# Kernel tuning notes

Hardware: AMD Instinct MI355X
Metric: run time of the kernel (lower is better)

Reference implementation:

```python
import jax, jax.numpy as jnp
import numpy as np

B, T, I, H, O = 4096, 256, 5, 64, 25


def _lstm_layer(x, Wih, Whh, bih, bhh):
    """One LSTM layer, batch_first. x: [B,T,in], Wih: [4H,in], Whh: [4H,H].
    PyTorch gate order: i, f, g, o."""
    b, t, _ = x.shape
    h_dim = Whh.shape[1]
    # Precompute input contribution for all timesteps: [B,T,4H]
    gx = jnp.einsum('bti,gi->btg', x, Wih) + bih + bhh

    def step(carry, g_t):
        h, c = carry
        gates = g_t + h @ Whh.T  # [B,4H]
        i, f, g, o = jnp.split(gates, 4, axis=-1)
        i = jax.nn.sigmoid(i)
        f = jax.nn.sigmoid(f)
        g = jnp.tanh(g)
        o = jax.nn.sigmoid(o)
        c = f * c + i * g
        h = o * jnp.tanh(c)
        return (h, c), h

    h0 = jnp.zeros((b, h_dim), x.dtype)
    (_, _), hs = jax.lax.scan(step, (h0, h0), jnp.swapaxes(gx, 0, 1))  # hs: [T,B,H]
    return jnp.swapaxes(hs, 0, 1)  # [B,T,H]


def setup_inputs() -> dict:
    key = jax.random.key(0)
    ks = jax.random.split(key, 12)
    k = 1.0 / np.sqrt(H)  # torch LSTM/Linear init scale
    u = lambda kk, shp: jax.random.uniform(kk, shp, jnp.float32, -k, k)
    return {
        'x': jax.random.normal(ks[0], (B, T, I), jnp.float32),
        'Wih0': u(ks[1], (4 * H, I)),
        'Whh0': u(ks[2], (4 * H, H)),
        'bih0': u(ks[3], (4 * H,)),
        'bhh0': u(ks[4], (4 * H,)),
        'Wih1': u(ks[5], (4 * H, H)),
        'Whh1': u(ks[6], (4 * H, H)),
        'bih1': u(ks[7], (4 * H,)),
        'bhh1': u(ks[8], (4 * H,)),
        'Wfc': u(ks[9], (O, H)),
        'bfc': u(ks[10], (O,)),
    }


def reference(x, Wih0, Whh0, bih0, bhh0, Wih1, Whh1, bih1, bhh1, Wfc, bfc):
    # 2-layer LSTM (dropout = identity in eval mode)
    h1 = _lstm_layer(x, Wih0, Whh0, bih0, bhh0)   # [B,T,H]
    h2 = _lstm_layer(h1, Wih1, Whh1, bih1, bhh1)  # [B,T,H]
    last = h2[:, -1, :]                            # [B,H]
    out = last @ Wfc.T + bfc                       # [B,25]
    return out.reshape(x.shape[0], 5, 5)
```

## Files before the change

### kernel.cpp

```cpp
#include <hip/hip_runtime.h>


#define TT   256
#define II   5
#define HH   64
#define OO   25
#define MT   16
#define NTHR 1024
#define XP   520
#define HSZ  1024
#define HF   65

typedef __attribute__((ext_vector_type(8))) short  short8;
typedef __attribute__((ext_vector_type(4))) float  floatx4;

#define MFMA(a, b, c) __builtin_amdgcn_mfma_f32_16x16x32_bf16(a, b, c, 0, 0, 0)

__device__ __forceinline__ float frcp(float x) { return __builtin_amdgcn_rcpf(x); }
__device__ __forceinline__ float fexp2(float x) { return __builtin_amdgcn_exp2f(x); }
__device__ __forceinline__ unsigned short bf16_rne(float f) {
    unsigned int u = __builtin_bit_cast(unsigned int, f);
    u += 0x7FFFu + ((u >> 16) & 1u);
    return (unsigned short)(u >> 16);
}
__device__ __forceinline__ float cell_update(const floatx4& g, float& c) {
    const float gi = frcp(1.f + fexp2(g[0]));
    const float gf = frcp(1.f + fexp2(g[1]));
    const float gz = fmaf(-2.f, frcp(1.f + fexp2(g[2])), 1.f);
    const float go = frcp(1.f + fexp2(g[3]));
    c = fmaf(gf, c, gi * gz);
    const float tc = fmaf(-2.f, frcp(1.f + fexp2(c * 2.885390082f)), 1.f);
    return go * tc;
}

__global__ __attribute__((amdgpu_flat_work_group_size(1024, 1024),
                          amdgpu_waves_per_eu(4, 4)))
void lstm_mfma9(const float* __restrict__ x,
                const float* __restrict__ Wih0, const float* __restrict__ Whh0,
                const float* __restrict__ bih0, const float* __restrict__ bhh0,
                const float* __restrict__ Wih1, const float* __restrict__ Whh1,
                const float* __restrict__ bih1, const float* __restrict__ bhh1,
                const float* __restrict__ Wfc,  const float* __restrict__ bfc,
                float* __restrict__ out)
{
    __shared__ __align__(16) unsigned short xhi[MT * XP];
    __shared__ __align__(16) unsigned short h1hi[2 * HSZ];
    __shared__ __align__(16) unsigned short h2hi[2 * HSZ];
    __shared__ __align__(16) float          h2f[MT * HF];

    const int tid   = threadIdx.x;
    const int w     = tid >> 6;
    const int lane  = tid & 63;
    const int b     = lane & 15;
    const int q     = lane >> 4;
    const int jmine = 4 * w + q;
    const int hw_off = ((jmine >> 3) * 16 + b) * 8 + (jmine & 7);
    const int ro     = lane * 8;

    short8 A1h[2];
    short8 A2h[4];
    short8 Axwh;
    {
        const int rr = lane & 15;
        const int g  = (rr & 3) * 64 + 4 * w + (rr >> 2);
        const float sc = ((rr & 3) == 2) ? 2.885390082f : -1.442695041f;
        #pragma unroll
        for (int c = 0; c < 2; ++c)
            #pragma unroll
            for (int jj = 0; jj < 8; ++jj)
                A1h[c][jj] = (short)bf16_rne(sc * Whh0[g * HH + c * 32 + q * 8 + jj]);
        #pragma unroll
        for (int c = 0; c < 4; ++c)
            #pragma unroll
            for (int jj = 0; jj < 8; ++jj) {
                const int k = c * 32 + q * 8 + jj;
                float wv = (k < HH) ? Wih1[g * HH + k] : Whh1[g * HH + (k - HH)];
                A2h[c][jj] = (short)bf16_rne(sc * wv);
            }
        #pragma unroll
        for (int jj = 0; jj < 8; ++jj) {
            const int k = q * 8 + jj;
            Axwh[jj] = (k < II) ? (short)bf16_rne(sc * Wih0[g * II + k]) : (short)0;
        }
    }
    float bias1[4], bias2[4];
    #pragma unroll
    for (int r = 0; r < 4; ++r) {
        const int g = r * 64 + jmine;
        const float sc = (r == 2) ? 2.885390082f : -1.442695041f;
        bias1[r] = sc * (bih0[g] + bhh0[g]);
        bias2[r] = sc * (bih1[g] + bhh1[g]);
    }

    for (int i = tid; i < MT * XP / 2; i += NTHR)
        ((unsigned int*)xhi)[i] = 0u;
    for (int i = tid; i < HSZ; i += NTHR) {
        ((unsigned int*)h1hi)[i] = 0u;
        ((unsigned int*)h2hi)[i] = 0u;
    }
    float c1 = 0.f, c2 = 0.f;
    __syncthreads();

    const int blockBase = blockIdx.x * MT;

    auto refill_x = [&](int t0) {
        const int rb = tid >> 6, dt = tid & 63;
        const float* src = x + ((size_t)(blockBase + rb) * TT + t0 + dt) * II;
        unsigned short* ph = xhi + rb * XP + dt * 8;
        #pragma unroll
        for (int ii = 0; ii < II; ++ii)
            ph[ii] = bf16_rne(src[ii]);
    };

    refill_x(0);
    __syncthreads();
    {
        short8 Bxh = *(const short8*)(xhi + b * XP);
        floatx4 a1 = {bias1[0], bias1[1], bias1[2], bias1[3]};
        a1 = MFMA(Axwh, Bxh, a1);
        const float h = cell_update(a1, c1);
        h1hi[0 * HSZ + hw_off] = bf16_rne(h);
    }
    __syncthreads();

    const unsigned short* xptr = xhi + b * XP + 8;

#define STEP_BODY(WP, RP)                                                     \
    {                                                                         \
        short8 H1h0 = *(const short8*)(h1hi + (WP) * HSZ + ro);               \
        short8 H1h1 = *(const short8*)(h1hi + (WP) * HSZ + 512 + ro);         \
        short8 H2h0 = *(const short8*)(h2hi + (RP) * HSZ + ro);               \
        short8 H2h1 = *(const short8*)(h2hi + (RP) * HSZ + 512 + ro);         \
        short8 Bxh  = *(const short8*)(xptr);                                 \
        xptr += 8;                                                            \
        floatx4 a2 = {bias2[0], bias2[1], bias2[2], bias2[3]};                \
        a2 = MFMA(A2h[0], H1h0, a2);                                          \
        a2 = MFMA(A2h[1], H1h1, a2);                                          \
        a2 = MFMA(A2h[2], H2h0, a2);                                          \
        a2 = MFMA(A2h[3], H2h1, a2);                                          \
        floatx4 a1 = {bias1[0], bias1[1], bias1[2], bias1[3]};                \
        a1 = MFMA(Axwh, Bxh, a1);                                             \
        a1 = MFMA(A1h[0], H1h0, a1);                                          \
        a1 = MFMA(A1h[1], H1h1, a1);                                          \
        {                                                                     \
            const float h = cell_update(a2, c2);                              \
            h2hi[(WP) * HSZ + hw_off] = bf16_rne(h);                          \
        }                                                                     \
        {                                                                     \
            const float h = cell_update(a1, c1);                              \
            h1hi[(RP) * HSZ + hw_off] = bf16_rne(h);                          \
        }                                                                     \
        __syncthreads();                                                      \
    }

    for (int i = 0; i < 254; i += 2) {
        STEP_BODY(0, 1)
        if (((i + 2) & 63) == 0) {
            refill_x(i + 2);
            xptr = xhi + b * XP;
            __syncthreads();
        }
        STEP_BODY(1, 0)
    }
    STEP_BODY(0, 1)
#undef STEP_BODY

    {
        short8 H1h0 = *(const short8*)(h1hi + 1 * HSZ + ro);
        short8 H1h1 = *(const short8*)(h1hi + 1 * HSZ + 512 + ro);
        short8 H2h0 = *(const short8*)(h2hi + 0 * HSZ + ro);
        short8 H2h1 = *(const short8*)(h2hi + 0 * HSZ + 512 + ro);
        floatx4 a2 = {bias2[0], bias2[1], bias2[2], bias2[3]};
        a2 = MFMA(A2h[0], H1h0, a2);
        a2 = MFMA(A2h[1], H1h1, a2);
        a2 = MFMA(A2h[2], H2h0, a2);
        a2 = MFMA(A2h[3], H2h1, a2);
        const float h = cell_update(a2, c2);
        h2f[b * HF + jmine] = h;
    }
    __syncthreads();

    if (tid < MT * OO) {
        const int bb = tid / OO, o = tid - bb * OO;
        float acc = bfc[o];
        const float* wr = Wfc + o * HH;
        const float* hr = h2f + bb * HF;
        #pragma unroll
        for (int j = 0; j < HH; ++j) acc += wr[j] * hr[j];
        out[((size_t)blockIdx.x * MT + bb) * OO + o] = acc;
    }
}

extern "C" void kernel_launch(void* const* d_in, const int* in_sizes, int n_in,
                              void* d_out, int out_size, void* d_ws, size_t ws_size,
                              hipStream_t stream) {
    const float* x    = (const float*)d_in[0];
    const float* Wih0 = (const float*)d_in[1];
    const float* Whh0 = (const float*)d_in[2];
    const float* bih0 = (const float*)d_in[3];
    const float* bhh0 = (const float*)d_in[4];
    const float* Wih1 = (const float*)d_in[5];
    const float* Whh1 = (const float*)d_in[6];
    const float* bih1 = (const float*)d_in[7];
    const float* bhh1 = (const float*)d_in[8];
    const float* Wfc  = (const float*)d_in[9];
    const float* bfc  = (const float*)d_in[10];
    float* out = (float*)d_out;

    dim3 grid(4096 / MT), block(NTHR);
    lstm_mfma9<<<grid, block, 0, stream>>>(x, Wih0, Whh0, bih0, bhh0,
                                           Wih1, Whh1, bih1, bhh1,
                                           Wfc, bfc, out);
}
```

Measured before the change: 259.8 us.

## Halve batch tile per block and give each wave two gate tiles

Shrinks each block to 8 batch rows and 512 threads, doubling the grid, so a CU can host two independent blocks whose recurrences interleave. Each wave now owns 8 hidden units and issues two interleaved MFMA chains. The 16-wide MFMA B operand carries the 8 batch rows twice, and each hidden value is written to both copies. The aim is cheaper 512-thread barriers and better latency hiding across blocks, in exchange for doubling total MFMA work, since half of each output tile is redundant.

```diff
diff --git a/kernel.cpp b/kernel.cpp
--- a/kernel.cpp
+++ b/kernel.cpp
@@ -5,8 +5,8 @@
 #define II   5
 #define HH   64
 #define OO   25
-#define MT   16
-#define NTHR 1024
+#define MT   8
+#define NTHR 512
 #define XP   520
 #define HSZ  1024
 #define HF   65
@@ -33,15 +33,15 @@
     return go * tc;
 }
 
-__global__ __attribute__((amdgpu_flat_work_group_size(1024, 1024),
+__global__ __attribute__((amdgpu_flat_work_group_size(512, 512),
                           amdgpu_waves_per_eu(4, 4)))
-void lstm_mfma9(const float* __restrict__ x,
-                const float* __restrict__ Wih0, const float* __restrict__ Whh0,
-                const float* __restrict__ bih0, const float* __restrict__ bhh0,
-                const float* __restrict__ Wih1, const float* __restrict__ Whh1,
-                const float* __restrict__ bih1, const float* __restrict__ bhh1,
-                const float* __restrict__ Wfc,  const float* __restrict__ bfc,
-                float* __restrict__ out)
+void lstm_mfma10(const float* __restrict__ x,
+                 const float* __restrict__ Wih0, const float* __restrict__ Whh0,
+                 const float* __restrict__ bih0, const float* __restrict__ bhh0,
+                 const float* __restrict__ Wih1, const float* __restrict__ Whh1,
+                 const float* __restrict__ bih1, const float* __restrict__ bhh1,
+                 const float* __restrict__ Wfc,  const float* __restrict__ bfc,
+                 float* __restrict__ out)
 {
     __shared__ __align__(16) unsigned short xhi[MT * XP];
     __shared__ __align__(16) unsigned short h1hi[2 * HSZ];
@@ -51,45 +51,50 @@
     const int tid   = threadIdx.x;
     const int w     = tid >> 6;
     const int lane  = tid & 63;
-    const int b     = lane & 15;
+    const int b8    = lane & 7;
     const int q     = lane >> 4;
-    const int jmine = 4 * w + q;
-    const int hw_off = ((jmine >> 3) * 16 + b) * 8 + (jmine & 7);
-    const int ro     = lane * 8;
-
-    short8 A1h[2];
-    short8 A2h[4];
-    short8 Axwh;
+    const int sel   = (lane >> 3) & 1;
+    const bool low  = (sel == 0);
+    const int jmine = 8 * w + 4 * sel + q;
+    const int hw_off = w * 128 + b8 * 8 + 4 * sel + q;
+    const int ro8    = (q * 16 + b8) * 8;
+
+    short8 A1h[2][2];
+    short8 A2h[2][4];
+    short8 Axwh[2];
     {
         const int rr = lane & 15;
-        const int g  = (rr & 3) * 64 + 4 * w + (rr >> 2);
         const float sc = ((rr & 3) == 2) ? 2.885390082f : -1.442695041f;
         #pragma unroll
-        for (int c = 0; c < 2; ++c)
+        for (int s = 0; s < 2; ++s) {
+            const int g = (rr & 3) * 64 + 8 * w + 4 * s + (rr >> 2);
             #pragma unroll
-            for (int jj = 0; jj < 8; ++jj)
-                A1h[c][jj] = (short)bf16_rne(sc * Whh0[g * HH + c * 32 + q * 8 + jj]);
-        #pragma unroll
-        for (int c = 0; c < 4; ++c)
+            for (int c = 0; c < 2; ++c)
+                #pragma unroll
+                for (int jj = 0; jj < 8; ++jj)
+                    A1h[s][c][jj] = (short)bf16_rne(sc * Whh0[g * HH + c * 32 + q * 8 + jj]);
+            #pragma unroll
+            for (int c = 0; c < 4; ++c)
+                #pragma unroll
+                for (int jj = 0; jj < 8; ++jj) {
+                    const int k = c * 32 + q * 8 + jj;
+                    float wv = (k < HH) ? Wih1[g * HH + k] : Whh1[g * HH + (k - HH)];
+                    A2h[s][c][jj] = (short)bf16_rne(sc * wv);
+                }
             #pragma unroll
             for (int jj = 0; jj < 8; ++jj) {
-                const int k = c * 32 + q * 8 + jj;
-                float wv = (k < HH) ? Wih1[g * HH + k] : Whh1[g * HH + (k - HH)];
-                A2h[c][jj] = (short)bf16_rne(sc * wv);
+                const int k = q * 8 + jj;
+                Axwh[s][jj] = (k < II) ? (short)bf16_rne(sc * Wih0[g * II + k]) : (short)0;
             }
-        #pragma unroll
-        for (int jj = 0; jj < 8; ++jj) {
-            const int k = q * 8 + jj;
-            Axwh[jj] = (k < II) ? (short)bf16_rne(sc * Wih0[g * II + k]) : (short)0;
         }
     }
-    float bias1[4], bias2[4];
+    floatx4 bias1v, bias2v;
     #pragma unroll
     for (int r = 0; r < 4; ++r) {
         const int g = r * 64 + jmine;
         const float sc = (r == 2) ? 2.885390082f : -1.442695041f;
-        bias1[r] = sc * (bih0[g] + bhh0[g]);
-        bias2[r] = sc * (bih1[g] + bhh1[g]);
+        bias1v[r] = sc * (bih0[g] + bhh0[g]);
+        bias2v[r] = sc * (bih1[g] + bhh1[g]);
     }
 
     for (int i = tid; i < MT * XP / 2; i += NTHR)
@@ -115,40 +120,59 @@
     refill_x(0);
     __syncthreads();
     {
-        short8 Bxh = *(const short8*)(xhi + b * XP);
-        floatx4 a1 = {bias1[0], bias1[1], bias1[2], bias1[3]};
-        a1 = MFMA(Axwh, Bxh, a1);
-        const float h = cell_update(a1, c1);
-        h1hi[0 * HSZ + hw_off] = bf16_rne(h);
-    }
-    __syncthreads();
-
-    const unsigned short* xptr = xhi + b * XP + 8;
+        short8 Bxh = *(const short8*)(xhi + b8 * XP);
+        floatx4 a1t0 = MFMA(Axwh[0], Bxh, bias1v);
+        floatx4 a1t1 = MFMA(Axwh[1], Bxh, bias1v);
+        floatx4 a1m;
+        #pragma unroll
+        for (int r = 0; r < 4; ++r) a1m[r] = low ? a1t0[r] : a1t1[r];
+        const float h = cell_update(a1m, c1);
+        const unsigned short hv = bf16_rne(h);
+        h1hi[0 * HSZ + hw_off]      = hv;
+        h1hi[0 * HSZ + hw_off + 64] = hv;
+    }
+    __syncthreads();
+
+    const unsigned short* xptr = xhi + b8 * XP + 8;
 
 #define STEP_BODY(WP, RP)                                                     \
     {                                                                         \
-        short8 H1h0 = *(const short8*)(h1hi + (WP) * HSZ + ro);               \
-        short8 H1h1 = *(const short8*)(h1hi + (WP) * HSZ + 512 + ro);         \
-        short8 H2h0 = *(const short8*)(h2hi + (RP) * HSZ + ro);               \
-        short8 H2h1 = *(const short8*)(h2hi + (RP) * HSZ + 512 + ro);         \
+        short8 H1h0 = *(const short8*)(h1hi + (WP) * HSZ + ro8);              \
+        short8 H1h1 = *(const short8*)(h1hi + (WP) * HSZ + 512 + ro8);        \
+        short8 H2h0 = *(const short8*)(h2hi + (RP) * HSZ + ro8);              \
+        short8 H2h1 = *(const short8*)(h2hi + (RP) * HSZ + 512 + ro8);        \
         short8 Bxh  = *(const short8*)(xptr);                                 \
         xptr += 8;                                                            \
-        floatx4 a2 = {bias2[0], bias2[1], bias2[2], bias2[3]};                \
-        a2 = MFMA(A2h[0], H1h0, a2);                                          \
-        a2 = MFMA(A2h[1], H1h1, a2);                                          \
-        a2 = MFMA(A2h[2], H2h0, a2);                                          \
-        a2 = MFMA(A2h[3], H2h1, a2);                                          \
-        floatx4 a1 = {bias1[0], bias1[1], bias1[2], bias1[3]};                \
-        a1 = MFMA(Axwh, Bxh, a1);                                             \
-        a1 = MFMA(A1h[0], H1h0, a1);                                          \
-        a1 = MFMA(A1h[1], H1h1, a1);                                          \
+        floatx4 a2t0 = MFMA(A2h[0][0], H1h0, bias2v);                         \
+        floatx4 a2t1 = MFMA(A2h[1][0], H1h0, bias2v);                         \
+        a2t0 = MFMA(A2h[0][1], H1h1, a2t0);                                   \
+        a2t1 = MFMA(A2h[1][1], H1h1, a2t1);                                   \
+        a2t0 = MFMA(A2h[0][2], H2h0, a2t0);                                   \
+        a2t1 = MFMA(A2h[1][2], H2h0, a2t1);                                   \
+        a2t0 = MFMA(A2h[0][3], H2h1, a2t0);                                   \
+        a2t1 = MFMA(A2h[1][3], H2h1, a2t1);                                   \
+        floatx4 a1t0 = MFMA(Axwh[0], Bxh, bias1v);                            \
+        floatx4 a1t1 = MFMA(Axwh[1], Bxh, bias1v);                            \
+        a1t0 = MFMA(A1h[0][0], H1h0, a1t0);                                   \
+        a1t1 = MFMA(A1h[1][0], H1h0, a1t1);                                   \
+        a1t0 = MFMA(A1h[0][1], H1h1, a1t0);                                   \
+        a1t1 = MFMA(A1h[1][1], H1h1, a1t1);                                   \
+        floatx4 a2m, a1m;                                                     \
+        _Pragma("unroll")                                                     \
+        for (int r = 0; r < 4; ++r) a2m[r] = low ? a2t0[r] : a2t1[r];         \
+        _Pragma("unroll")                                                     \
+        for (int r = 0; r < 4; ++r) a1m[r] = low ? a1t0[r] : a1t1[r];         \
         {                                                                     \
-            const float h = cell_update(a2, c2);                              \
-            h2hi[(WP) * HSZ + hw_off] = bf16_rne(h);                          \
+            const float h = cell_update(a2m, c2);                             \
+            const unsigned short hv = bf16_rne(h);                            \
+            h2hi[(WP) * HSZ + hw_off]      = hv;                              \
+            h2hi[(WP) * HSZ + hw_off + 64] = hv;                              \
         }                                                                     \
         {                                                                     \
-            const float h = cell_update(a1, c1);                              \
-            h1hi[(RP) * HSZ + hw_off] = bf16_rne(h);                          \
+            const float h = cell_update(a1m, c1);                             \
+            const unsigned short hv = bf16_rne(h);                            \
+            h1hi[(RP) * HSZ + hw_off]      = hv;                              \
+            h1hi[(RP) * HSZ + hw_off + 64] = hv;                              \
         }                                                                     \
         __syncthreads();                                                      \
     }
@@ -157,7 +181,7 @@
         STEP_BODY(0, 1)
         if (((i + 2) & 63) == 0) {
             refill_x(i + 2);
-            xptr = xhi + b * XP;
+            xptr = xhi + b8 * XP;
             __syncthreads();
         }
         STEP_BODY(1, 0)
@@ -166,17 +190,23 @@
 #undef STEP_BODY
 
     {
-        short8 H1h0 = *(const short8*)(h1hi + 1 * HSZ + ro);
-        short8 H1h1 = *(const short8*)(h1hi + 1 * HSZ + 512 + ro);
-        short8 H2h0 = *(const short8*)(h2hi + 0 * HSZ + ro);
-        short8 H2h1 = *(const short8*)(h2hi + 0 * HSZ + 512 + ro);
-        floatx4 a2 = {bias2[0], bias2[1], bias2[2], bias2[3]};
-        a2 = MFMA(A2h[0], H1h0, a2);
-        a2 = MFMA(A2h[1], H1h1, a2);
-        a2 = MFMA(A2h[2], H2h0, a2);
-        a2 = MFMA(A2h[3], H2h1, a2);
-        const float h = cell_update(a2, c2);
-        h2f[b * HF + jmine] = h;
+        short8 H1h0 = *(const short8*)(h1hi + 1 * HSZ + ro8);
+        short8 H1h1 = *(const short8*)(h1hi + 1 * HSZ + 512 + ro8);
+        short8 H2h0 = *(const short8*)(h2hi + 0 * HSZ + ro8);
+        short8 H2h1 = *(const short8*)(h2hi + 0 * HSZ + 512 + ro8);
+        floatx4 a2t0 = MFMA(A2h[0][0], H1h0, bias2v);
+        floatx4 a2t1 = MFMA(A2h[1][0], H1h0, bias2v);
+        a2t0 = MFMA(A2h[0][1], H1h1, a2t0);
+        a2t1 = MFMA(A2h[1][1], H1h1, a2t1);
+        a2t0 = MFMA(A2h[0][2], H2h0, a2t0);
+        a2t1 = MFMA(A2h[1][2], H2h0, a2t1);
+        a2t0 = MFMA(A2h[0][3], H2h1, a2t0);
+        a2t1 = MFMA(A2h[1][3], H2h1, a2t1);
+        floatx4 a2m;
+        #pragma unroll
+        for (int r = 0; r < 4; ++r) a2m[r] = low ? a2t0[r] : a2t1[r];
+        const float h = cell_update(a2m, c2);
+        h2f[b8 * HF + jmine] = h;
     }
     __syncthreads();
 
@@ -208,7 +238,7 @@
     float* out = (float*)d_out;
 
     dim3 grid(4096 / MT), block(NTHR);
-    lstm_mfma9<<<grid, block, 0, stream>>>(x, Wih0, Whh0, bih0, bhh0,
-                                           Wih1, Whh1, bih1, bhh1,
-                                           Wfc, bfc, out);
-}
+    lstm_mfma10<<<grid, block, 0, stream>>>(x, Wih0, Whh0, bih0, bhh0,
+                                            Wih1, Whh1, bih1, bhh1,
+                                            Wfc, bfc, out);
+}
```

After: 329.0 us. 1.27x slower.

## Halve batch tile and split MFMA columns between LSTM layers

Applied to the files above, without the earlier changes.

Reduces the batch tile per block from 16 to 8 rows, doubling the grid, and maps the 16 MFMA columns so half the lanes do layer-1 cell updates and half do layer-2. Each lane now runs a single cell_update per step instead of two, which shortens the per-step serial transcendental chain. Waves-per-EU is raised to 8 so two blocks can share a CU. In exchange, half of each MFMA's columns carry duplicated batch data, so per-sample matrix work doubles and there are twice as many blocks, each running the full 256-step barrier chain.

```diff
diff --git a/kernel.cpp b/kernel.cpp
--- a/kernel.cpp
+++ b/kernel.cpp
@@ -5,10 +5,10 @@
 #define II   5
 #define HH   64
 #define OO   25
-#define MT   16
+#define MT   8
 #define NTHR 1024
 #define XP   520
-#define HSZ  1024
+#define HSZ  512
 #define HF   65
 
 typedef __attribute__((ext_vector_type(8))) short  short8;
@@ -34,14 +34,14 @@
 }
 
 __global__ __attribute__((amdgpu_flat_work_group_size(1024, 1024),
-                          amdgpu_waves_per_eu(4, 4)))
-void lstm_mfma9(const float* __restrict__ x,
-                const float* __restrict__ Wih0, const float* __restrict__ Whh0,
-                const float* __restrict__ bih0, const float* __restrict__ bhh0,
-                const float* __restrict__ Wih1, const float* __restrict__ Whh1,
-                const float* __restrict__ bih1, const float* __restrict__ bhh1,
-                const float* __restrict__ Wfc,  const float* __restrict__ bfc,
-                float* __restrict__ out)
+                          amdgpu_waves_per_eu(8, 8)))
+void lstm_mfma11(const float* __restrict__ x,
+                 const float* __restrict__ Wih0, const float* __restrict__ Whh0,
+                 const float* __restrict__ bih0, const float* __restrict__ bhh0,
+                 const float* __restrict__ Wih1, const float* __restrict__ Whh1,
+                 const float* __restrict__ bih1, const float* __restrict__ bhh1,
+                 const float* __restrict__ Wfc,  const float* __restrict__ bfc,
+                 float* __restrict__ out)
 {
     __shared__ __align__(16) unsigned short xhi[MT * XP];
     __shared__ __align__(16) unsigned short h1hi[2 * HSZ];
@@ -51,11 +51,13 @@
     const int tid   = threadIdx.x;
     const int w     = tid >> 6;
     const int lane  = tid & 63;
-    const int b     = lane & 15;
+    const int b8    = lane & 7;
     const int q     = lane >> 4;
+    const int sel   = (lane >> 3) & 1;
+    const bool isl2 = (sel != 0);
     const int jmine = 4 * w + q;
-    const int hw_off = ((jmine >> 3) * 16 + b) * 8 + (jmine & 7);
-    const int ro     = lane * 8;
+    const int hw_base = ((jmine >> 3) * 8 + b8) * 8 + (jmine & 7);
+    const int ro8     = (q * 8 + b8) * 8;
 
     short8 A1h[2];
     short8 A2h[4];
@@ -83,100 +85,102 @@
             Axwh[jj] = (k < II) ? (short)bf16_rne(sc * Wih0[g * II + k]) : (short)0;
         }
     }
-    float bias1[4], bias2[4];
+    floatx4 bias1v, bias2v;
     #pragma unroll
     for (int r = 0; r < 4; ++r) {
         const int g = r * 64 + jmine;
         const float sc = (r == 2) ? 2.885390082f : -1.442695041f;
-        bias1[r] = sc * (bih0[g] + bhh0[g]);
-        bias2[r] = sc * (bih1[g] + bhh1[g]);
+        bias1v[r] = sc * (bih0[g] + bhh0[g]);
+        bias2v[r] = sc * (bih1[g] + bhh1[g]);
     }
 
     for (int i = tid; i < MT * XP / 2; i += NTHR)
         ((unsigned int*)xhi)[i] = 0u;
-    for (int i = tid; i < HSZ; i += NTHR) {
-        ((unsigned int*)h1hi)[i] = 0u;
-        ((unsigned int*)h2hi)[i] = 0u;
-    }
-    float c1 = 0.f, c2 = 0.f;
+    if (tid < HSZ) {
+        ((unsigned int*)h1hi)[tid] = 0u;
+        ((unsigned int*)h2hi)[tid] = 0u;
+    }
+    float c1 = 0.f;
     __syncthreads();
 
     const int blockBase = blockIdx.x * MT;
 
     auto refill_x = [&](int t0) {
-        const int rb = tid >> 6, dt = tid & 63;
-        const float* src = x + ((size_t)(blockBase + rb) * TT + t0 + dt) * II;
-        unsigned short* ph = xhi + rb * XP + dt * 8;
-        #pragma unroll
-        for (int ii = 0; ii < II; ++ii)
-            ph[ii] = bf16_rne(src[ii]);
+        if (tid < 512) {
+            const int rb = tid >> 6, dt = tid & 63;
+            const float* src = x + ((size_t)(blockBase + rb) * TT + t0 + dt) * II;
+            unsigned short* ph = xhi + rb * XP + dt * 8;
+            #pragma unroll
+            for (int ii = 0; ii < II; ++ii)
+                ph[ii] = bf16_rne(src[ii]);
+        }
     };
 
     refill_x(0);
     __syncthreads();
     {
-        short8 Bxh = *(const short8*)(xhi + b * XP);
-        floatx4 a1 = {bias1[0], bias1[1], bias1[2], bias1[3]};
-        a1 = MFMA(Axwh, Bxh, a1);
-        const float h = cell_update(a1, c1);
-        h1hi[0 * HSZ + hw_off] = bf16_rne(h);
-    }
-    __syncthreads();
-
-    const unsigned short* xptr = xhi + b * XP + 8;
-
-#define STEP_BODY(WP, RP)                                                     \
+        short8 Bxh = *(const short8*)(xhi + b8 * XP);
+        floatx4 a1 = MFMA(Axwh, Bxh, bias1v);
+        if (!isl2) {
+            const float h = cell_update(a1, c1);
+            h1hi[hw_base] = bf16_rne(h);
+        }
+    }
+    __syncthreads();
+
+    unsigned short* const wptrE = isl2 ? (h2hi + hw_base) : (h1hi + HSZ + hw_base);
+    unsigned short* const wptrO = isl2 ? (h2hi + HSZ + hw_base) : (h1hi + hw_base);
+
+    const unsigned short* xptr = xhi + b8 * XP + 8;
+
+#define STEP_BODY(WP, RP, WPTR)                                               \
     {                                                                         \
-        short8 H1h0 = *(const short8*)(h1hi + (WP) * HSZ + ro);               \
-        short8 H1h1 = *(const short8*)(h1hi + (WP) * HSZ + 512 + ro);         \
-        short8 H2h0 = *(const short8*)(h2hi + (RP) * HSZ + ro);               \
-        short8 H2h1 = *(const short8*)(h2hi + (RP) * HSZ + 512 + ro);         \
+        short8 H1h0 = *(const short8*)(h1hi + (WP) * HSZ + ro8);              \
+        short8 H1h1 = *(const short8*)(h1hi + (WP) * HSZ + 256 + ro8);        \
+        short8 H2h0 = *(const short8*)(h2hi + (RP) * HSZ + ro8);              \
+        short8 H2h1 = *(const short8*)(h2hi + (RP) * HSZ + 256 + ro8);        \
         short8 Bxh  = *(const short8*)(xptr);                                 \
         xptr += 8;                                                            \
-        floatx4 a2 = {bias2[0], bias2[1], bias2[2], bias2[3]};                \
-        a2 = MFMA(A2h[0], H1h0, a2);                                          \
+        floatx4 a2 = MFMA(A2h[0], H1h0, bias2v);                              \
         a2 = MFMA(A2h[1], H1h1, a2);                                          \
         a2 = MFMA(A2h[2], H2h0, a2);                                          \
         a2 = MFMA(A2h[3], H2h1, a2);                                          \
-        floatx4 a1 = {bias1[0], bias1[1], bias1[2], bias1[3]};                \
-        a1 = MFMA(Axwh, Bxh, a1);                                             \
+        floatx4 a1 = MFMA(Axwh, Bxh, bias1v);                                 \
         a1 = MFMA(A1h[0], H1h0, a1);                                          \
         a1 = MFMA(A1h[1], H1h1, a1);                                          \
-        {                                                                     \
-            const float h = cell_update(a2, c2);                              \
-            h2hi[(WP) * HSZ + hw_off] = bf16_rne(h);                          \
-        }                                                                     \
-        {                                                                     \
-            const float h = cell_update(a1, c1);                              \
-            h1hi[(RP) * HSZ + hw_off] = bf16_rne(h);                          \
-        }                                                                     \
+        floatx4 g;                                                            \
+        _Pragma("unroll")                                                     \
+        for (int r = 0; r < 4; ++r) g[r] = isl2 ? a2[r] : a1[r];              \
+        const float h = cell_update(g, c1);                                   \
+        *(WPTR) = bf16_rne(h);                                                \
         __syncthreads();                                                      \
     }
 
     for (int i = 0; i < 254; i += 2) {
-        STEP_BODY(0, 1)
+        STEP_BODY(0, 1, wptrE)
         if (((i + 2) & 63) == 0) {
             refill_x(i + 2);
-            xptr = xhi + b * XP;
+            xptr = xhi + b8 * XP;
             __syncthreads();
         }
-        STEP_BODY(1, 0)
-    }
-    STEP_BODY(0, 1)
+        STEP_BODY(1, 0, wptrO)
+    }
+    STEP_BODY(0, 1, wptrE)
 #undef STEP_BODY
 
     {
-        short8 H1h0 = *(const short8*)(h1hi + 1 * HSZ + ro);
-        short8 H1h1 = *(const short8*)(h1hi + 1 * HSZ + 512 + ro);
-        short8 H2h0 = *(const short8*)(h2hi + 0 * HSZ + ro);
-        short8 H2h1 = *(const short8*)(h2hi + 0 * HSZ + 512 + ro);
-        floatx4 a2 = {bias2[0], bias2[1], bias2[2], bias2[3]};
-        a2 = MFMA(A2h[0], H1h0, a2);
+        short8 H1h0 = *(const short8*)(h1hi + 1 * HSZ + ro8);
+        short8 H1h1 = *(const short8*)(h1hi + 1 * HSZ + 256 + ro8);
+        short8 H2h0 = *(const short8*)(h2hi + 0 * HSZ + ro8);
+        short8 H2h1 = *(const short8*)(h2hi + 0 * HSZ + 256 + ro8);
+        floatx4 a2 = MFMA(A2h[0], H1h0, bias2v);
         a2 = MFMA(A2h[1], H1h1, a2);
         a2 = MFMA(A2h[2], H2h0, a2);
         a2 = MFMA(A2h[3], H2h1, a2);
-        const float h = cell_update(a2, c2);
-        h2f[b * HF + jmine] = h;
+        if (isl2) {
+            const float h = cell_update(a2, c1);
+            h2f[b8 * HF + jmine] = h;
+        }
     }
     __syncthreads();
 
@@ -208,7 +212,7 @@
     float* out = (float*)d_out;
 
     dim3 grid(4096 / MT), block(NTHR);
-    lstm_mfma9<<<grid, block, 0, stream>>>(x, Wih0, Whh0, bih0, bhh0,
-                                           Wih1, Whh1, bih1, bhh1,
-                                           Wfc, bfc, out);
-}
+    lstm_mfma11<<<grid, block, 0, stream>>>(x, Wih0, Whh0, bih0, bhh0,
+                                            Wih1, Whh1, bih1, bhh1,
+                                            Wfc, bfc, out);
+}
```

Result: slower. 337.0 us (+29.7%).
